# Performance work log

Hardware: AMD Instinct MI355X
Metric: run time of the kernel (lower is better)

The kernel has to match this reference:

```python
import jax, jax.numpy as jnp
import numpy as np

EMBED_DIM = 128


def setup_inputs() -> dict:
    key = jax.random.key(0)
    k = jax.random.split(key, 6)
    B, S, H, D = 4, 512, 768, EMBED_DIM
    ent_embeddings = jax.random.normal(k[0], (B, S, H), jnp.float32)
    ent_type_ids = jax.random.randint(k[1], (B, S), 0, 10)  # entity-type labels (>=0)
    ent_mask = jax.random.randint(k[2], (B, S), 0, 2)       # 0/1 attention mask
    W_mu = jax.random.normal(k[3], (H, D), jnp.float32) / np.sqrt(H)
    b_mu = jnp.zeros((D,), jnp.float32)
    W_sigma = jax.random.normal(k[4], (H, D), jnp.float32) / np.sqrt(H)
    b_sigma = jnp.zeros((D,), jnp.float32)
    return dict(ent_embeddings=ent_embeddings, ent_type_ids=ent_type_ids, ent_mask=ent_mask,
                W_mu=W_mu, b_mu=b_mu, W_sigma=W_sigma, b_sigma=b_sigma)


def _pairwise_kl(mu, sigma, dim):
    # Symmetrized KL between diagonal Gaussians for all pairs (i=row, j=col).
    # Decomposed into rank-D contractions instead of materializing [N,N,D].
    inv = 1.0 / sigma                               # [N,D]
    S_log = jnp.sum(jnp.log(sigma), axis=1)         # [N] sum_d log sigma (1e-14 inside log is negligible in fp32)
    A = jnp.einsum('id,jd->ij', inv, sigma)         # sum_d sigma_j/sigma_i
    q = jnp.sum(mu * mu * inv, axis=1)              # [N] sum_d mu_i^2/sigma_i
    cross = jnp.einsum('id,jd->ij', mu * inv, mu)   # sum_d mu_i*mu_j/sigma_i
    quad = jnp.einsum('id,jd->ij', inv, mu * mu)    # sum_d mu_j^2/sigma_i
    md_i = q[:, None] - 2.0 * cross + quad          # sum_d (mu_i-mu_j)^2 / sigma_i
    ld = S_log[None, :] - S_log[:, None]            # sum_d log(sigma_j/sigma_i)
    ij_kl = 0.5 * (A + md_i - dim - ld)
    ji_kl = 0.5 * (A.T + md_i.T - dim + ld)
    return 0.5 * (ij_kl + ji_kl)


def reference(ent_embeddings, ent_type_ids, ent_mask, W_mu, b_mu, W_sigma, b_sigma):
    D = EMBED_DIM
    h = jax.nn.relu(ent_embeddings)                 # dropout in eval mode (identity)
    mu = (h @ W_mu + b_mu).reshape(-1, D)           # [N,D]
    sigma = (jax.nn.elu(h @ W_sigma + b_sigma) + 1.0 + 1e-14).reshape(-1, D)

    labels = ent_type_ids.reshape(-1)
    valid = (ent_mask.reshape(-1) == 1) & (labels >= 0)   # consider_mutual_O=True: no labels>0 filter

    # loss_mask: ALL coordinates of mu differ (kills diagonal / duplicate rows)
    alldiff = jnp.all(mu[:, None, :] != mu[None, :, :], axis=-1)  # [N,N]
    pair_valid = valid[:, None] & valid[None, :]
    lab_eq = labels[:, None] == labels[None, :]
    denom_m = (alldiff & pair_valid).astype(mu.dtype)             # loss_mask
    num_w = (lab_eq & alldiff & pair_valid).astype(mu.dtype)      # loss_weights

    loss = -_pairwise_kl(mu, sigma, D)              # loss_type='KL'

    # NT-Xent, temperature=1
    e = jnp.exp(loss)
    cnts = jnp.sum(num_w, axis=1)
    loss_num = jnp.sum(e * num_w, axis=1)
    loss_den = jnp.sum(e * denom_m, axis=1)
    sel = cnts > 0
    safe = lambda v: jnp.where(sel, v, 1.0)
    lf = -jnp.log2(safe(loss_num)) + jnp.log2(safe(loss_den)) + jnp.log2(safe(cnts))
    n_sel = jnp.maximum(jnp.sum(sel.astype(mu.dtype)), 1.0)
    return jnp.sum(jnp.where(sel, lf, 0.0)) / n_sel
```

## Files before the change

kernel.cpp:

```cpp
#include <hip/hip_runtime.h>
#include <math.h>

#define NROWS 2048
#define HDIM 768
#define DDIM 128
#define FEAT 512
#define DCAP 2048
#define TSLOTS 8192

typedef __attribute__((ext_vector_type(8))) short bf16x8;
typedef __attribute__((ext_vector_type(4))) float f32x4;

__device__ __forceinline__ void mergeState(float& m, float& n, float& d,
                                           float m2, float n2, float d2) {
  float M = fmaxf(m, m2);
  float s1 = (m >= M) ? 1.0f : __expf(m - M);
  float s2 = (m2 >= M) ? 1.0f : __expf(m2 - M);
  n = n * s1 + n2 * s2;
  d = d * s1 + d2 * s2;
  m = M;
}

__device__ __forceinline__ unsigned short bfhi(float x) {
  unsigned int u = __float_as_uint(x);
  return (unsigned short)((u + 0x7fffu + ((u >> 16) & 1u)) >> 16);
}

__global__ __launch_bounds__(256) void k1m(
    const float* __restrict__ E, const float* __restrict__ Wmu,
    const float* __restrict__ Wsg, float* __restrict__ Cpart,
    unsigned long long* __restrict__ tab, int* __restrict__ rowflag,
    int* __restrict__ dupcnt, float* __restrict__ gsum)
{
  __shared__ unsigned short lds[12288];
  const int t = threadIdx.x;
  const int bid = blockIdx.x;

  if (t < 32) tab[bid * 32 + t] = 0ULL;
  if (t < 8)  rowflag[bid * 8 + t] = 0;
  if (bid == 0 && t == 0) {
    dupcnt[0] = 0;
    gsum[0] = 0.f; gsum[1] = 0.f; gsum[2] = 0.f;
  }

  const int mt = bid & 31, nt = (bid >> 5) & 1, ks = bid >> 6;
  const int i0 = mt * 64, kbase = ks * 192;
  const float* Wsrc = nt ? Wsg : Wmu;

  const int akg = t & 3, arow = t >> 2;
  const int bcol = t & 127, bkh = t >> 7;
  const int aw  = akg * 512 + arow * 8;
  const int bw0 = 2048 + (bkh * 2) * 1024 + bcol * 8;
  const int bw1 = bw0 + 1024;

  float4 rA0, rA1; float rB[16];

  auto loadRegs = [&](int it) {
    const int ka = kbase + it * 32;
    const float* ep = E + (size_t)(i0 + arow) * HDIM + ka + akg * 8;
    rA0 = *reinterpret_cast<const float4*>(ep);
    rA1 = *reinterpret_cast<const float4*>(ep + 4);
    const float* wp = Wsrc + (size_t)(ka + bkh * 16) * DDIM + bcol;
    #pragma unroll
    for (int j = 0; j < 16; ++j) rB[j] = wp[(size_t)j * DDIM];
  };

  auto writeLds = [&](int buf) {
    unsigned short* lb = lds + buf * 6144;
    unsigned short ha[8];
    ha[0] = bfhi(fmaxf(rA0.x, 0.f)); ha[1] = bfhi(fmaxf(rA0.y, 0.f));
    ha[2] = bfhi(fmaxf(rA0.z, 0.f)); ha[3] = bfhi(fmaxf(rA0.w, 0.f));
    ha[4] = bfhi(fmaxf(rA1.x, 0.f)); ha[5] = bfhi(fmaxf(rA1.y, 0.f));
    ha[6] = bfhi(fmaxf(rA1.z, 0.f)); ha[7] = bfhi(fmaxf(rA1.w, 0.f));
    *reinterpret_cast<ushort4*>(lb + aw)     = make_ushort4(ha[0], ha[1], ha[2], ha[3]);
    *reinterpret_cast<ushort4*>(lb + aw + 4) = make_ushort4(ha[4], ha[5], ha[6], ha[7]);
    unsigned short hb[16];
    #pragma unroll
    for (int j = 0; j < 16; ++j) hb[j] = bfhi(rB[j]);
    *reinterpret_cast<ushort4*>(lb + bw0)     = make_ushort4(hb[0],  hb[1],  hb[2],  hb[3]);
    *reinterpret_cast<ushort4*>(lb + bw0 + 4) = make_ushort4(hb[4],  hb[5],  hb[6],  hb[7]);
    *reinterpret_cast<ushort4*>(lb + bw1)     = make_ushort4(hb[8],  hb[9],  hb[10], hb[11]);
    *reinterpret_cast<ushort4*>(lb + bw1 + 4) = make_ushort4(hb[12], hb[13], hb[14], hb[15]);
  };

  f32x4 acc[2][4];
  #pragma unroll
  for (int a = 0; a < 2; ++a)
    #pragma unroll
    for (int b = 0; b < 4; ++b) {
      acc[a][b][0] = 0.f; acc[a][b][1] = 0.f; acc[a][b][2] = 0.f; acc[a][b][3] = 0.f;
    }

  const int wid = t >> 6, lane = t & 63;
  const int wr = wid >> 1, wc = wid & 1;
  const int gq = lane >> 4, c0 = lane & 15;

  loadRegs(0);
  writeLds(0);
  loadRegs(1);
  __syncthreads();

  for (int it = 0; it < 6; ++it) {
    {
      const unsigned short* lb = lds + (it & 1) * 6144;
      bf16x8 ah[2], bh[4];
      #pragma unroll
      for (int fa = 0; fa < 2; ++fa) {
        const int ia = gq * 512 + (wr * 32 + fa * 16 + c0) * 8;
        ah[fa] = *reinterpret_cast<const bf16x8*>(lb + ia);
      }
      #pragma unroll
      for (int fb = 0; fb < 4; ++fb) {
        const int ib = 2048 + gq * 1024 + (wc * 64 + fb * 16 + c0) * 8;
        bh[fb] = *reinterpret_cast<const bf16x8*>(lb + ib);
      }
      #pragma unroll
      for (int fa = 0; fa < 2; ++fa)
        #pragma unroll
        for (int fb = 0; fb < 4; ++fb)
          acc[fa][fb] = __builtin_amdgcn_mfma_f32_16x16x32_bf16(
              ah[fa], bh[fb], acc[fa][fb], 0, 0, 0);
    }
    if (it < 5) {
      writeLds((it + 1) & 1);
      if (it < 4) loadRegs(it + 2);
    }
    __syncthreads();
  }

  const int n0 = nt * 128;
  #pragma unroll
  for (int fa = 0; fa < 2; ++fa)
    #pragma unroll
    for (int fb = 0; fb < 4; ++fb)
      #pragma unroll
      for (int r = 0; r < 4; ++r) {
        const int row = i0 + wr * 32 + fa * 16 + gq * 4 + r;
        const int col = n0 + wc * 64 + fb * 16 + c0;
        Cpart[((size_t)ks * NROWS + row) * 256 + col] = acc[fa][fb][r];
      }
}

__global__ __launch_bounds__(256) void k1e(
    const float* __restrict__ Cpart, const float* __restrict__ bmu,
    const float* __restrict__ bsg,
    unsigned short* __restrict__ Ftl,
    float* __restrict__ qout, unsigned long long* __restrict__ tab,
    int* __restrict__ rowflag, int* __restrict__ dupcnt,
    int2* __restrict__ duplist)
{
  __shared__ unsigned short fbuf[16][520];
  const int t = threadIdx.x;
  const int row16 = t >> 4, cw = t & 15, c8 = cw * 8;
  const int g = blockIdx.x;
  const int rg = g * 16 + row16;

  float vm[8], vs[8];
  #pragma unroll
  for (int j = 0; j < 8; ++j) { vm[j] = 0.f; vs[j] = 0.f; }
  #pragma unroll
  for (int ks = 0; ks < 4; ++ks) {
    const float* src = &Cpart[((size_t)ks * NROWS + rg) * 256];
    float4 m0 = *reinterpret_cast<const float4*>(src + c8);
    float4 m1 = *reinterpret_cast<const float4*>(src + c8 + 4);
    float4 s0 = *reinterpret_cast<const float4*>(src + 128 + c8);
    float4 s1 = *reinterpret_cast<const float4*>(src + 128 + c8 + 4);
    vm[0] += m0.x; vm[1] += m0.y; vm[2] += m0.z; vm[3] += m0.w;
    vm[4] += m1.x; vm[5] += m1.y; vm[6] += m1.z; vm[7] += m1.w;
    vs[0] += s0.x; vs[1] += s0.y; vs[2] += s0.z; vs[3] += s0.w;
    vs[4] += s1.x; vs[5] += s1.y; vs[6] += s1.z; vs[7] += s1.w;
  }

  float q = 0.f;
  unsigned int hx = 0u, hs2 = 0u;
  unsigned short o1[8], o2[8], o3[8], o4[8];
  #pragma unroll
  for (int j = 0; j < 8; ++j) {
    const int col = c8 + j;
    float z = vs[j] + bsg[col];
    float s = (z > 0.f ? z + 1.0f : __expf(z)) + 1e-14f;
    float mu = vm[j] + bmu[col];
    float inv = 1.0f / s;
    o1[j] = bfhi(inv);
    o2[j] = bfhi(s + mu * mu);
    o3[j] = bfhi(-2.0f * mu * inv);
    o4[j] = bfhi(mu);
    q += mu * mu * inv;
    unsigned int b = __float_as_uint(mu);
    if (b == 0x80000000u) b = 0u;
    unsigned int hm = (b ^ ((unsigned int)col * 0x9E3779B9u)) * 0x85EBCA6Bu;
    hm ^= hm >> 13;
    hx ^= hm;
    hs2 += hm * 0xC2B2AE35u;
  }
  *reinterpret_cast<ushort4*>(&fbuf[row16][      c8])     = make_ushort4(o1[0], o1[1], o1[2], o1[3]);
  *reinterpret_cast<ushort4*>(&fbuf[row16][      c8 + 4]) = make_ushort4(o1[4], o1[5], o1[6], o1[7]);
  *reinterpret_cast<ushort4*>(&fbuf[row16][128 + c8])     = make_ushort4(o2[0], o2[1], o2[2], o2[3]);
  *reinterpret_cast<ushort4*>(&fbuf[row16][128 + c8 + 4]) = make_ushort4(o2[4], o2[5], o2[6], o2[7]);
  *reinterpret_cast<ushort4*>(&fbuf[row16][256 + c8])     = make_ushort4(o3[0], o3[1], o3[2], o3[3]);
  *reinterpret_cast<ushort4*>(&fbuf[row16][256 + c8 + 4]) = make_ushort4(o3[4], o3[5], o3[6], o3[7]);
  *reinterpret_cast<ushort4*>(&fbuf[row16][384 + c8])     = make_ushort4(o4[0], o4[1], o4[2], o4[3]);
  *reinterpret_cast<ushort4*>(&fbuf[row16][384 + c8 + 4]) = make_ushort4(o4[4], o4[5], o4[6], o4[7]);

  #pragma unroll
  for (int o = 8; o; o >>= 1) q += __shfl_xor(q, o, 16);
  #pragma unroll
  for (int o = 1; o < 16; o <<= 1) {
    hx  ^= (unsigned int)__shfl_xor((int)hx, o, 16);
    hs2 += (unsigned int)__shfl_xor((int)hs2, o, 16);
  }
  if (cw == 0) {
    qout[rg] = q;
    unsigned long long key = (((unsigned long long)hx << 32) | hs2) & ~0xFFFULL;
    if (key == 0ULL) key = 0x123456789000ULL;
    const unsigned long long me = key | (unsigned long long)(rg + 1);
    unsigned int h = (hx ^ (hs2 * 0x9E3779B9u)) & (TSLOTS - 1);
    for (;;) {
      unsigned long long old = atomicCAS(&tab[h], 0ULL, me);
      if (old == 0ULL) break;
      if ((old & ~0xFFFULL) == key) {
        int r2 = (int)(old & 0xFFFULL) - 1;
        rowflag[rg] = 1; rowflag[r2] = 1;
        int e = atomicAdd(dupcnt, 1);
        if (e < DCAP) duplist[e] = make_int2(min(rg, r2), max(rg, r2));
      }
      h = (h + 1u) & (TSLOTS - 1);
    }
  }
  __syncthreads();

  #pragma unroll
  for (int u = 0; u < 4; ++u) {
    const int f = u * 256 + t;
    const int kb = f >> 6, ln = f & 63;
    const int gq2 = ln >> 4, cc = ln & 15;
    uint4 v = *reinterpret_cast<const uint4*>(&fbuf[cc][kb * 32 + gq2 * 8]);
    *reinterpret_cast<uint4*>(&Ftl[((size_t)(g * 16 + kb)) * 512 + ln * 8]) = v;
  }
}

__global__ __launch_bounds__(512, 2) void k2_mfma(
    const unsigned short* __restrict__ Ftl,
    const float* __restrict__ qv, const int* __restrict__ labels,
    const int* __restrict__ msk, const int* __restrict__ rowflag,
    const int* __restrict__ dupcnt, const int2* __restrict__ duplist,
    float4* __restrict__ ipart)
{
  __shared__ unsigned short Blds[32768];
  const int t = threadIdx.x;
  const int orig = blockIdx.x;
  const int xcd = orig & 7, idx = orig >> 3;
  const int bi = (xcd >> 1) * 4 + (idx >> 4);
  const int bj = (xcd & 1) * 16 + (idx & 15);
  const int i0 = bi * 128, j0 = bj * 64;
  const int wid = t >> 6, lane = t & 63;
  const int wr = wid >> 1, wc = wid & 1;
  const int gq = lane >> 4, c0 = lane & 15;

  {
    const unsigned short* Bsrc = Ftl + (size_t)bj * 32768;
    #pragma unroll
    for (int u = 0; u < 8; ++u) {
      const int slot = u * 512 + t;
      uint4 v = *reinterpret_cast<const uint4*>(Bsrc + slot * 8);
      *reinterpret_cast<uint4*>(Blds + slot * 8) = v;
    }
  }
  __syncthreads();

  const int ga0 = bi * 8 + wr * 2;
  const unsigned short* fl = Ftl + lane * 8;
  const unsigned short* bl = Blds + lane * 8;
  const int hb0 = wc * 2;

  f32x4 acc[2][2];
  #pragma unroll
  for (int a = 0; a < 2; ++a)
    #pragma unroll
    for (int b = 0; b < 2; ++b) {
      acc[a][b][0] = 0.f; acc[a][b][1] = 0.f; acc[a][b][2] = 0.f; acc[a][b][3] = 0.f;
    }

  bf16x8 Abuf[3][2];

#define LOADA(kb_, s_)                                                         \
  {                                                                            \
    Abuf[s_][0] = *reinterpret_cast<const bf16x8*>(fl + ((ga0    ) * 16 + (kb_)) * 512); \
    Abuf[s_][1] = *reinterpret_cast<const bf16x8*>(fl + ((ga0 + 1) * 16 + (kb_)) * 512); \
  }

#define STEP(kb_, s_)                                                          \
  {                                                                            \
    const int kbb_ = (kb_) ^ 4;                                                \
    bf16x8 B0 = *reinterpret_cast<const bf16x8*>(bl + ((hb0    ) * 16 + kbb_) * 512); \
    bf16x8 B1 = *reinterpret_cast<const bf16x8*>(bl + ((hb0 + 1) * 16 + kbb_) * 512); \
    acc[0][0] = __builtin_amdgcn_mfma_f32_16x16x32_bf16(Abuf[s_][0], B0, acc[0][0], 0, 0, 0); \
    acc[0][1] = __builtin_amdgcn_mfma_f32_16x16x32_bf16(Abuf[s_][0], B1, acc[0][1], 0, 0, 0); \
    acc[1][0] = __builtin_amdgcn_mfma_f32_16x16x32_bf16(Abuf[s_][1], B0, acc[1][0], 0, 0, 0); \
    acc[1][1] = __builtin_amdgcn_mfma_f32_16x16x32_bf16(Abuf[s_][1], B1, acc[1][1], 0, 0, 0); \
  }

  LOADA(0, 0);
  LOADA(1, 1);
  #pragma unroll
  for (int kb = 0; kb < 16; ++kb) {
    if (kb < 14) { LOADA(kb + 2, (kb + 2) % 3); }
    STEP(kb, kb % 3);
  }
#undef LOADA
#undef STEP

  const int ndup = min(dupcnt[0], DCAP);
  int ljv[2]; float qjv[2]; int fjv[2]; int gjv[2];
  #pragma unroll
  for (int fb = 0; fb < 2; ++fb) {
    const int gj = j0 + wc * 32 + fb * 16 + c0;
    const int lab = labels[gj];
    ljv[fb] = (msk[gj] == 1 && lab >= 0) ? lab : -1;
    qjv[fb] = qv[gj];
    fjv[fb] = rowflag[gj];
    gjv[fb] = gj;
  }
  #pragma unroll
  for (int fa = 0; fa < 2; ++fa) {
    const int ibase = i0 + wr * 32 + fa * 16 + gq * 4;
    int li4[4], mi4[4], fi4[4]; float qi4[4];
    *reinterpret_cast<int4*>(li4)   = *reinterpret_cast<const int4*>(labels + ibase);
    *reinterpret_cast<int4*>(mi4)   = *reinterpret_cast<const int4*>(msk + ibase);
    *reinterpret_cast<int4*>(fi4)   = *reinterpret_cast<const int4*>(rowflag + ibase);
    *reinterpret_cast<float4*>(qi4) = *reinterpret_cast<const float4*>(qv + ibase);
    #pragma unroll
    for (int r = 0; r < 4; ++r) {
      const int gi = ibase + r;
      const int li = (mi4[r] == 1 && li4[r] >= 0) ? li4[r] : -1;
      float m = -INFINITY, n = 0.f, d = 0.f, c = 0.f;
      if (li >= 0) {
        #pragma unroll
        for (int fb = 0; fb < 2; ++fb) {
          const int lj = ljv[fb];
          bool inc = (lj >= 0) && (gi != gjv[fb]);
          if (inc && fi4[r] && fjv[fb]) {
            int plo = min(gi, gjv[fb]), phi = max(gi, gjv[fb]);
            for (int e = 0; e < ndup; ++e) {
              int2 p = duplist[e];
              if (p.x == plo && p.y == phi) { inc = false; break; }
            }
          }
          if (inc) {
            float S = acc[fa][fb][r];
            float l = 64.0f - 0.25f * (qi4[r] + qjv[fb] + S);
            float w = (li == lj) ? 1.0f : 0.0f;
            mergeState(m, n, d, l, w, 1.0f);
            c += w;
          }
        }
      }
      #pragma unroll
      for (int o = 1; o < 16; o <<= 1) {
        float m2 = __shfl_xor(m, o);
        float n2 = __shfl_xor(n, o);
        float d2 = __shfl_xor(d, o);
        float c2 = __shfl_xor(c, o);
        mergeState(m, n, d, m2, n2, d2);
        c += c2;
      }
      if (c0 == 0)
        ipart[(size_t)(bj * 2 + wc) * NROWS + gi] = make_float4(m, n, d, c);
    }
  }
}

__global__ __launch_bounds__(256) void k3(const float4* __restrict__ ipart,
                                          float* __restrict__ gsum,
                                          float* __restrict__ out)
{
  const int r = blockIdx.x * 256 + threadIdx.x;
  float m = -INFINITY, n = 0.f, d = 0.f, c = 0.f;
  #pragma unroll 8
  for (int js = 0; js < 64; ++js) {
    float4 p = ipart[(size_t)js * NROWS + r];
    mergeState(m, n, d, p.x, p.y, p.z);
    c += p.w;
  }
  float lf = 0.f, ns = 0.f;
  if (c > 0.f) {
    lf = log2f(d) - log2f(n) + log2f(c);
    ns = 1.f;
  }
  #pragma unroll
  for (int o = 32; o; o >>= 1) {
    lf += __shfl_down(lf, o);
    ns += __shfl_down(ns, o);
  }
  __shared__ float sl[4], sn[4];
  const int wid = threadIdx.x >> 6;
  if ((threadIdx.x & 63) == 0) { sl[wid] = lf; sn[wid] = ns; }
  __syncthreads();
  if (threadIdx.x == 0) {
    float L = sl[0] + sl[1] + sl[2] + sl[3];
    float C = sn[0] + sn[1] + sn[2] + sn[3];
    atomicAdd(&gsum[0], L);
    atomicAdd(&gsum[1], C);
    __threadfence();
    unsigned int tk = atomicAdd(reinterpret_cast<unsigned int*>(gsum + 2), 1u);
    if (tk == 7u) {
      float Lt = atomicAdd(&gsum[0], 0.f);
      float Ct = atomicAdd(&gsum[1], 0.f);
      out[0] = Lt / fmaxf(Ct, 1.0f);
    }
  }
}

extern "C" void kernel_launch(void* const* d_in, const int* in_sizes, int n_in,
                              void* d_out, int out_size, void* d_ws, size_t ws_size,
                              hipStream_t stream) {
  const float* E   = (const float*)d_in[0];
  const int*   tid = (const int*)d_in[1];
  const int*   msk = (const int*)d_in[2];
  const float* Wmu = (const float*)d_in[3];
  const float* bmu = (const float*)d_in[4];
  const float* Wsg = (const float*)d_in[5];
  const float* bsg = (const float*)d_in[6];

  unsigned char* w = (unsigned char*)d_ws;
  unsigned short* Ftl  = (unsigned short*)w;  w += (size_t)NROWS * FEAT * 2;
  float* Cpart         = (float*)w;           w += (size_t)4 * NROWS * 256 * 4;
  float* qv            = (float*)w;           w += (size_t)NROWS * 4;
  unsigned long long* tab = (unsigned long long*)w; w += (size_t)TSLOTS * 8;
  int* rowflag         = (int*)w;             w += (size_t)NROWS * 4;
  int* dupcnt          = (int*)w;             w += 256;
  float* gsum          = (float*)w;           w += 256;
  int2* duplist        = (int2*)w;            w += (size_t)DCAP * 8;
  float4* ipart        = (float4*)w;          w += (size_t)64 * NROWS * 16;

  k1m<<<256, 256, 0, stream>>>(E, Wmu, Wsg, Cpart, tab, rowflag, dupcnt, gsum);
  k1e<<<128, 256, 0, stream>>>(Cpart, bmu, bsg, Ftl, qv,
                               tab, rowflag, dupcnt, duplist);
  k2_mfma<<<512, 512, 0, stream>>>(Ftl, qv, tid, msk, rowflag,
                                   dupcnt, duplist, ipart);
  k3<<<8, 256, 0, stream>>>(ipart, gsum, (float*)d_out);
}
```

Measured before the change: 44.51 us.

## Stage A operand tiles through double-buffered LDS instead of per-wave global loads

In the MFMA Gram kernel, each wave previously loaded its A fragments straight from global memory with a 3-deep register prefetch. The two waves sharing a row group therefore fetched the same data twice. Now the block cooperatively loads the 128-row A tile in four k-chunks into a double-buffered LDS region, with register staging one chunk ahead. This cuts redundant global traffic but doubles shared memory to 128 KB per block, which may limit occupancy under launch_bounds(512,2), and adds a barrier per chunk.

After: 65.43 us. +47.0%, slower.

```diff
diff --git a/kernel.cpp b/kernel.cpp
--- a/kernel.cpp
+++ b/kernel.cpp
@@ -247,6 +247,7 @@
     float4* __restrict__ ipart)
 {
   __shared__ unsigned short Blds[32768];
+  __shared__ unsigned short Alds[32768];
   const int t = threadIdx.x;
   const int orig = blockIdx.x;
   const int xcd = orig & 7, idx = orig >> 3;
@@ -266,12 +267,28 @@
       *reinterpret_cast<uint4*>(Blds + slot * 8) = v;
     }
   }
-  __syncthreads();
-
-  const int ga0 = bi * 8 + wr * 2;
-  const unsigned short* fl = Ftl + lane * 8;
+
   const unsigned short* bl = Blds + lane * 8;
   const int hb0 = wc * 2;
+  uint4 sreg[4];
+
+  auto stageRegs = [&](int s) {
+    #pragma unroll
+    for (int u = 0; u < 4; ++u) {
+      const int fi = u * 8 + wid;
+      const int g = fi >> 2, kbo = fi & 3;
+      sreg[u] = *reinterpret_cast<const uint4*>(
+          Ftl + ((size_t)((bi * 8 + g) * 16 + 4 * s + kbo)) * 512 + lane * 8);
+    }
+  };
+  auto writeA = [&](int s) {
+    unsigned short* ab = Alds + (s & 1) * 16384;
+    #pragma unroll
+    for (int u = 0; u < 4; ++u) {
+      const int fi = u * 8 + wid;
+      *reinterpret_cast<uint4*>(ab + fi * 512 + lane * 8) = sreg[u];
+    }
+  };
 
   f32x4 acc[2][2];
   #pragma unroll
@@ -281,34 +298,36 @@
       acc[a][b][0] = 0.f; acc[a][b][1] = 0.f; acc[a][b][2] = 0.f; acc[a][b][3] = 0.f;
     }
 
-  bf16x8 Abuf[3][2];
-
-#define LOADA(kb_, s_)                                                         \
-  {                                                                            \
-    Abuf[s_][0] = *reinterpret_cast<const bf16x8*>(fl + ((ga0    ) * 16 + (kb_)) * 512); \
-    Abuf[s_][1] = *reinterpret_cast<const bf16x8*>(fl + ((ga0 + 1) * 16 + (kb_)) * 512); \
-  }
-
-#define STEP(kb_, s_)                                                          \
-  {                                                                            \
-    const int kbb_ = (kb_) ^ 4;                                                \
-    bf16x8 B0 = *reinterpret_cast<const bf16x8*>(bl + ((hb0    ) * 16 + kbb_) * 512); \
-    bf16x8 B1 = *reinterpret_cast<const bf16x8*>(bl + ((hb0 + 1) * 16 + kbb_) * 512); \
-    acc[0][0] = __builtin_amdgcn_mfma_f32_16x16x32_bf16(Abuf[s_][0], B0, acc[0][0], 0, 0, 0); \
-    acc[0][1] = __builtin_amdgcn_mfma_f32_16x16x32_bf16(Abuf[s_][0], B1, acc[0][1], 0, 0, 0); \
-    acc[1][0] = __builtin_amdgcn_mfma_f32_16x16x32_bf16(Abuf[s_][1], B0, acc[1][0], 0, 0, 0); \
-    acc[1][1] = __builtin_amdgcn_mfma_f32_16x16x32_bf16(Abuf[s_][1], B1, acc[1][1], 0, 0, 0); \
-  }
-
-  LOADA(0, 0);
-  LOADA(1, 1);
-  #pragma unroll
-  for (int kb = 0; kb < 16; ++kb) {
-    if (kb < 14) { LOADA(kb + 2, (kb + 2) % 3); }
-    STEP(kb, kb % 3);
-  }
-#undef LOADA
-#undef STEP
+  stageRegs(0);
+  writeA(0);
+  stageRegs(1);
+  __syncthreads();
+
+  for (int s = 0; s < 4; ++s) {
+    {
+      const unsigned short* ab = Alds + (s & 1) * 16384;
+      #pragma unroll
+      for (int kbo = 0; kbo < 4; ++kbo) {
+        const int kb = 4 * s + kbo;
+        const int kbb = kb ^ 4;
+        bf16x8 A0 = *reinterpret_cast<const bf16x8*>(
+            ab + ((wr * 2 + 0) * 4 + kbo) * 512 + lane * 8);
+        bf16x8 A1 = *reinterpret_cast<const bf16x8*>(
+            ab + ((wr * 2 + 1) * 4 + kbo) * 512 + lane * 8);
+        bf16x8 B0 = *reinterpret_cast<const bf16x8*>(bl + ((hb0    ) * 16 + kbb) * 512);
+        bf16x8 B1 = *reinterpret_cast<const bf16x8*>(bl + ((hb0 + 1) * 16 + kbb) * 512);
+        acc[0][0] = __builtin_amdgcn_mfma_f32_16x16x32_bf16(A0, B0, acc[0][0], 0, 0, 0);
+        acc[0][1] = __builtin_amdgcn_mfma_f32_16x16x32_bf16(A0, B1, acc[0][1], 0, 0, 0);
+        acc[1][0] = __builtin_amdgcn_mfma_f32_16x16x32_bf16(A1, B0, acc[1][0], 0, 0, 0);
+        acc[1][1] = __builtin_amdgcn_mfma_f32_16x16x32_bf16(A1, B1, acc[1][1], 0, 0, 0);
+      }
+    }
+    if (s < 3) {
+      writeA(s + 1);
+      if (s < 2) stageRegs(s + 2);
+    }
+    __syncthreads();
+  }
 
   const int ndup = min(dupcnt[0], DCAP);
   int ljv[2]; float qjv[2]; int fjv[2]; int gjv[2];
```
